# Performance work log

Hardware: AMD Instinct MI355X
Metric: run time of the kernel (lower is better)

The kernel has to match this reference:

```python
import jax, jax.numpy as jnp
import numpy as np

NUM_LOC = 20000
T = 24
IN_DIM = 18
H1 = 32
H2 = 32
GRU = 32
PW = 15
E_RAND = 640000


def setup_inputs() -> dict:
    key = jax.random.key(0)
    ks = jax.random.split(key, 32)
    # graph: random edges + self loops so every node has >=1 incoming edge
    edge_src = jnp.concatenate([
        jax.random.randint(ks[0], (E_RAND,), 0, NUM_LOC),
        jnp.arange(NUM_LOC)]).astype(jnp.int32)
    edge_dst = jnp.concatenate([
        jax.random.randint(ks[1], (E_RAND,), 0, NUM_LOC),
        jnp.arange(NUM_LOC)]).astype(jnp.int32)
    dynamic = jax.random.normal(ks[2], (NUM_LOC, T, IN_DIM), dtype=jnp.float32)
    cI = jax.random.uniform(ks[3], (T,), dtype=jnp.float32)
    cR = jax.random.uniform(ks[4], (T,), dtype=jnp.float32)
    I = jax.random.uniform(ks[5], (T,), dtype=jnp.float32)
    R = jax.random.uniform(ks[6], (T,), dtype=jnp.float32)
    N = jax.random.uniform(ks[7], (NUM_LOC, 1), dtype=jnp.float32) * 1e4 + 10.0
    h0 = jax.random.normal(ks[8], (1, GRU), dtype=jnp.float32) * 0.1
    s = 0.1
    # GAT layer 1 (torch Linear convention: weight [out, in], y = x @ W.T + b)
    W1 = jax.random.normal(ks[9], (H1, IN_DIM), dtype=jnp.float32) * s
    b1 = jnp.zeros((H1,), dtype=jnp.float32)
    aW1 = jax.random.normal(ks[10], (1, 2 * H1), dtype=jnp.float32) * s
    ab1 = jnp.zeros((1,), dtype=jnp.float32)
    # GAT layer 2
    W2 = jax.random.normal(ks[11], (H2, H1), dtype=jnp.float32) * s
    b2 = jnp.zeros((H2,), dtype=jnp.float32)
    aW2 = jax.random.normal(ks[12], (1, 2 * H2), dtype=jnp.float32) * s
    ab2 = jnp.zeros((1,), dtype=jnp.float32)
    # GRUCell
    Wih = jax.random.normal(ks[13], (3 * GRU, H2), dtype=jnp.float32) * s
    Whh = jax.random.normal(ks[14], (3 * GRU, GRU), dtype=jnp.float32) * s
    bih = jnp.zeros((3 * GRU,), dtype=jnp.float32)
    bhh = jnp.zeros((3 * GRU,), dtype=jnp.float32)
    # output heads
    WI = jax.random.normal(ks[15], (PW, GRU + 2), dtype=jnp.float32) * s
    bI = jnp.zeros((PW,), dtype=jnp.float32)
    WR = jax.random.normal(ks[16], (PW, GRU + 2), dtype=jnp.float32) * s
    bR = jnp.zeros((PW,), dtype=jnp.float32)
    Ws = jax.random.normal(ks[17], (2, GRU + 2), dtype=jnp.float32) * s
    bs = jnp.zeros((2,), dtype=jnp.float32)
    return {"dynamic": dynamic, "cI": cI, "cR": cR, "N": N, "I": I, "R": R,
            "h0": h0, "W1": W1, "b1": b1, "aW1": aW1, "ab1": ab1,
            "W2": W2, "b2": b2, "aW2": aW2, "ab2": ab2,
            "Wih": Wih, "Whh": Whh, "bih": bih, "bhh": bhh,
            "WI": WI, "bI": bI, "WR": WR, "bR": bR, "Ws": Ws, "bs": bs,
            "edge_src": edge_src, "edge_dst": edge_dst}


def _gat(x, W, b, aW, ab, src, dst):
    # z = fc(x); per-edge attention e = leaky_relu(attn_fc([z_src, z_dst]))
    z = x @ W.T + b                                        # [n, out]
    e = jax.nn.leaky_relu(
        (jnp.concatenate([z[src], z[dst]], axis=1) @ aW.T + ab)[:, 0])  # [E]
    # softmax over incoming edges per destination node
    m = jax.ops.segment_max(e, dst, num_segments=NUM_LOC)
    ex = jnp.exp(e - m[dst])
    den = jax.ops.segment_sum(ex, dst, num_segments=NUM_LOC)
    alpha = ex / den[dst]
    return jax.ops.segment_sum(alpha[:, None] * z[src], dst, num_segments=NUM_LOC)


def reference(dynamic, cI, cR, N, I, R, h0,
              W1, b1, aW1, ab1, W2, b2, aW2, ab2,
              Wih, Whh, bih, bhh, WI, bI, WR, bR, Ws, bs,
              edge_src, edge_dst):
    Nv = N[:, 0]                                          # [num_loc]

    def step(h, inp):
        x_t, cI_t, cR_t, I_t, R_t = inp
        c = jax.nn.elu(_gat(x_t, W1, b1, aW1, ab1, edge_src, edge_dst))
        c = jax.nn.elu(_gat(c, W2, b2, aW2, ab2, edge_src, edge_dst))
        pooled = jnp.max(c, axis=0)[None, :]              # [1, H2]
        # GRUCell
        gi = pooled @ Wih.T + bih
        gh = h @ Whh.T + bhh
        r = jax.nn.sigmoid(gi[:, :GRU] + gh[:, :GRU])
        zg = jax.nn.sigmoid(gi[:, GRU:2 * GRU] + gh[:, GRU:2 * GRU])
        n = jnp.tanh(gi[:, 2 * GRU:] + r * gh[:, 2 * GRU:])
        h_new = (1.0 - zg) * n + zg * h                   # [1, GRU]
        hc = jnp.concatenate([h_new, cI_t.reshape(1, 1), cR_t.reshape(1, 1)], axis=1)
        pred_I = hc @ WI.T + bI                           # [1, PW]
        pred_R = hc @ WR.T + bR
        sir = hc @ Ws.T + bs                              # [1, 2]
        alpha = jax.nn.sigmoid(sir[0, 0])
        beta = jax.nn.sigmoid(sir[0, 1])

        def sir_step(carry, _):
            lI, lR = carry
            lS = Nv - lI - lR
            dI = alpha * lI * (lS / Nv) - beta * lI
            dR = beta * lI
            return (lI + jax.lax.stop_gradient(dI),
                    lR + jax.lax.stop_gradient(dR)), (dI, dR)

        init = (jnp.broadcast_to(I_t, Nv.shape), jnp.broadcast_to(R_t, Nv.shape))
        _, (dIs, dRs) = jax.lax.scan(sir_step, init, None, length=PW)
        # [PW, num_loc] -> [num_loc, PW]
        return h_new, (pred_I, pred_R, dIs.T, dRs.T)

    xs = (jnp.swapaxes(dynamic, 0, 1), cI, cR, I, R)      # time-major
    h_fin, (nI, nR, pI, pR) = jax.lax.scan(step, h0, xs)
    new_I = jnp.transpose(nI, (1, 0, 2))                  # [1, T, PW]
    new_R = jnp.transpose(nR, (1, 0, 2))
    phy_I = jnp.transpose(pI, (1, 0, 2))                  # [num_loc, T, PW]
    phy_R = jnp.transpose(pR, (1, 0, 2))
    return new_I, new_R, phy_I, phy_R, h_fin
```

## Files before the change

kernel.cpp:

```cpp
#include <hip/hip_runtime.h>
#include <hip/hip_fp16.h>
#include <math.h>
#include <float.h>

#define NLOC 20000
#define TT   24
#define NP   12
#define INDIM 18
#define HH   32
#define PWN  15
#define PSTR 32

typedef unsigned short u16;

__device__ __forceinline__ unsigned int fkey(float f) {
    unsigned int b = __float_as_uint(f);
    return b ^ ((unsigned int)((int)b >> 31) | 0x80000000u);
}
__device__ __forceinline__ float funkey(unsigned int u) {
    return (u & 0x80000000u) ? __uint_as_float(u ^ 0x80000000u) : __uint_as_float(~u);
}

__device__ __forceinline__ bool decode_q(int nblk, int swz, int qadd,
                                         int& q, int& blk) {
    if (swz) {
        int F = blockIdx.x;
        int g = F >> 3;
        q = (F & 7) + 8 * (g / nblk);
        blk = g % nblk;
        return q < NP;
    }
    q = qadd + blockIdx.y;
    blk = blockIdx.x;
    return true;
}

__global__ void count_kernel(const int* __restrict__ dst, int* __restrict__ cnt, int E) {
    int e = blockIdx.x * blockDim.x + threadIdx.x;
    if (e < E) atomicAdd(&cnt[dst[e]], 1);
}

__global__ void scan_kernel(const int* __restrict__ cnt, int* __restrict__ row_ptr, int n) {
    __shared__ int sums[1024];
    const int CH = 20;
    int tid = threadIdx.x;
    int base = tid * CH;
    int local[CH];
    int s = 0;
    #pragma unroll
    for (int i = 0; i < CH; ++i) {
        int idx = base + i;
        int v = (idx < n) ? cnt[idx] : 0;
        local[i] = s;
        s += v;
    }
    sums[tid] = s;
    __syncthreads();
    for (int o = 1; o < 1024; o <<= 1) {
        int v = (tid >= o) ? sums[tid - o] : 0;
        __syncthreads();
        sums[tid] += v;
        __syncthreads();
    }
    int pre = (tid > 0) ? sums[tid - 1] : 0;
    #pragma unroll
    for (int i = 0; i < CH; ++i) {
        int idx = base + i;
        if (idx < n) row_ptr[idx] = pre + local[i];
    }
    if (tid == 1023) row_ptr[n] = sums[1023];
}

__global__ void scatter_kernel(const int* __restrict__ src, const int* __restrict__ dst,
                               const int* __restrict__ row_ptr, int* __restrict__ fill,
                               u16* __restrict__ csr_src, int E) {
    int e = blockIdx.x * blockDim.x + threadIdx.x;
    if (e < E) {
        int d = dst[e];
        int pos = row_ptr[d] + atomicAdd(&fill[d], 1);
        csr_src[pos] = (u16)src[e];
    }
}

__global__ void node1_kernel(const float* __restrict__ dyn,
                             const float* __restrict__ W, const float* __restrict__ b,
                             const float* __restrict__ aW, const float* __restrict__ ab,
                             __half2* __restrict__ z2, float2* __restrict__ es2,
                             float2* __restrict__ ed2, int nblk, int swz, int qadd) {
    __shared__ float sW[HH * INDIM];
    __shared__ float sb[HH];
    __shared__ float saW[2 * HH];
    __shared__ float sab;
    int q, blk;
    if (!decode_q(nblk, swz, qadd, q, blk)) return;
    int slice = swz ? q : blockIdx.y;
    int tid = threadIdx.x;
    for (int i = tid; i < HH * INDIM; i += blockDim.x) sW[i] = W[i];
    if (tid < HH) sb[tid] = b[tid];
    if (tid < 2 * HH) saW[tid] = aW[tid];
    if (tid == 0) sab = ab[0];
    __syncthreads();
    int n = blk * blockDim.x + tid;
    if (n >= NLOC) return;
    z2  += (size_t)slice * NLOC * HH;
    es2 += (size_t)slice * NLOC;
    ed2 += (size_t)slice * NLOC;
    const float* xp = dyn + (size_t)n * (TT * INDIM) + (size_t)(2 * q) * INDIM;
    float x0[INDIM], x1[INDIM];
    #pragma unroll
    for (int i = 0; i < INDIM; ++i) { x0[i] = xp[i]; x1[i] = xp[INDIM + i]; }
    float es0 = 0.f, es1 = 0.f, ed0 = sab, ed1 = sab;
    #pragma unroll
    for (int k = 0; k < HH; ++k) {
        float a0 = sb[k], a1 = sb[k];
        #pragma unroll
        for (int i = 0; i < INDIM; ++i) {
            a0 = fmaf(x0[i], sW[k * INDIM + i], a0);
            a1 = fmaf(x1[i], sW[k * INDIM + i], a1);
        }
        z2[(size_t)n * HH + k] = __floats2half2_rn(a0, a1);
        es0 = fmaf(saW[k], a0, es0);       es1 = fmaf(saW[k], a1, es1);
        ed0 = fmaf(saW[HH + k], a0, ed0);  ed1 = fmaf(saW[HH + k], a1, ed1);
    }
    es2[n] = make_float2(es0, es1);
    ed2[n] = make_float2(ed0, ed1);
}

__global__ void node2_kernel(const __half2* __restrict__ c2,
                             const float* __restrict__ W, const float* __restrict__ b,
                             const float* __restrict__ aW, const float* __restrict__ ab,
                             __half2* __restrict__ z2, float2* __restrict__ es2,
                             float2* __restrict__ ed2, int nblk, int swz, int qadd) {
    __shared__ float sW[HH * HH];
    __shared__ float sb[HH];
    __shared__ float saW[2 * HH];
    __shared__ float sab;
    int q, blk;
    if (!decode_q(nblk, swz, qadd, q, blk)) return;
    int slice = swz ? q : blockIdx.y;
    int tid = threadIdx.x;
    for (int i = tid; i < HH * HH; i += blockDim.x) sW[i] = W[i];
    if (tid < HH) sb[tid] = b[tid];
    if (tid < 2 * HH) saW[tid] = aW[tid];
    if (tid == 0) sab = ab[0];
    __syncthreads();
    int n = blk * blockDim.x + tid;
    if (n >= NLOC) return;
    c2  += (size_t)slice * NLOC * HH;
    z2  += (size_t)slice * NLOC * HH;
    es2 += (size_t)slice * NLOC;
    ed2 += (size_t)slice * NLOC;
    float x0[HH], x1[HH];
    const __half2* cp = c2 + (size_t)n * HH;
    #pragma unroll
    for (int i = 0; i < HH; ++i) {
        float2 f = __half22float2(cp[i]);
        x0[i] = f.x; x1[i] = f.y;
    }
    float es0 = 0.f, es1 = 0.f, ed0 = sab, ed1 = sab;
    #pragma unroll
    for (int k = 0; k < HH; ++k) {
        float a0 = sb[k], a1 = sb[k];
        #pragma unroll
        for (int i = 0; i < HH; ++i) {
            a0 = fmaf(x0[i], sW[k * HH + i], a0);
            a1 = fmaf(x1[i], sW[k * HH + i], a1);
        }
        z2[(size_t)n * HH + k] = __floats2half2_rn(a0, a1);
        es0 = fmaf(saW[k], a0, es0);       es1 = fmaf(saW[k], a1, es1);
        ed0 = fmaf(saW[HH + k], a0, ed0);  ed1 = fmaf(saW[HH + k], a1, ed1);
    }
    es2[n] = make_float2(es0, es1);
    ed2[n] = make_float2(ed0, ed1);
}

template<bool WRITE_C, bool POOL>
__global__ void __launch_bounds__(256, 4)
agg_kernel(const int* __restrict__ row_ptr, const u16* __restrict__ csr,
           const __half2* __restrict__ z2t, const float2* __restrict__ es2,
           const float2* __restrict__ ed2, __half2* __restrict__ c2out,
           unsigned int* __restrict__ pooled_u, int nblk, int swz, int qadd) {
    __shared__ int    soff[4][64];
    __shared__ float2 swt[4][64];
    __shared__ float  sred[4][2][HH];
    int q, dblk;
    if (!decode_q(nblk, swz, qadd, q, dblk)) return;
    int slice = swz ? q : blockIdx.y;
    int lane = threadIdx.x & 63;
    int w    = threadIdx.x >> 6;
    int r    = lane >> 3;
    int cg   = lane & 7;
    int d = dblk * 4 + w;
    const __half2* z2q  = z2t + (size_t)slice * NLOC * HH;
    const float2*  es2q = es2 + (size_t)slice * NLOC;
    const float2*  ed2q = ed2 + (size_t)slice * NLOC;

    int beg = 0, end = 0;
    float edd0 = 0.f, edd1 = 0.f;
    if (d < NLOC) {
        beg = row_ptr[d];
        end = row_ptr[d + 1];
        float2 ev = ed2q[d];
        edd0 = ev.x; edd1 = ev.y;
    }
    int deg = end - beg;
    int il = beg + lane;
    bool valid = (il < end);
    int idx_l = valid ? (int)csr[il] : 0;
    float2 esv = es2q[idx_l];
    float e0 = esv.x + edd0; e0 = fmaxf(e0, 0.01f * e0);
    float e1 = esv.y + edd1; e1 = fmaxf(e1, 0.01f * e1);
    float w0 = valid ? __expf(e0) : 0.f;
    float w1 = valid ? __expf(e1) : 0.f;
    soff[w][lane] = idx_l << 7;
    swt[w][lane]  = make_float2(w0, w1);

    const char* zb = (const char*)z2q + cg * 16;
    float2 ac0 = {0.f, 0.f}, ac1 = {0.f, 0.f}, ac2 = {0.f, 0.f}, ac3 = {0.f, 0.f};
    float den0 = 0.f, den1 = 0.f;
    #pragma unroll
    for (int pass = 0; pass < 8; ++pass) {
        int    off = soff[w][pass * 8 + r];
        float2 wv  = swt[w][pass * 8 + r];
        uint4 u = *(const uint4*)(zb + off);
        den0 += wv.x; den1 += wv.y;
        float2 f0 = __half22float2(*(const __half2*)&u.x);
        float2 f1 = __half22float2(*(const __half2*)&u.y);
        float2 f2 = __half22float2(*(const __half2*)&u.z);
        float2 f3 = __half22float2(*(const __half2*)&u.w);
        ac0.x = fmaf(wv.x, f0.x, ac0.x); ac0.y = fmaf(wv.y, f0.y, ac0.y);
        ac1.x = fmaf(wv.x, f1.x, ac1.x); ac1.y = fmaf(wv.y, f1.y, ac1.y);
        ac2.x = fmaf(wv.x, f2.x, ac2.x); ac2.y = fmaf(wv.y, f2.y, ac2.y);
        ac3.x = fmaf(wv.x, f3.x, ac3.x); ac3.y = fmaf(wv.y, f3.y, ac3.y);
    }
    for (int e = 64 + r; e < deg; e += 8) {
        int s2 = (int)csr[beg + e];
        float2 esv2 = es2q[s2];
        float t0 = esv2.x + edd0; t0 = fmaxf(t0, 0.01f * t0);
        float t1 = esv2.y + edd1; t1 = fmaxf(t1, 0.01f * t1);
        float x0 = __expf(t0), x1 = __expf(t1);
        den0 += x0; den1 += x1;
        uint4 u = *(const uint4*)(zb + ((size_t)s2 << 7));
        float2 f0 = __half22float2(*(const __half2*)&u.x);
        float2 f1 = __half22float2(*(const __half2*)&u.y);
        float2 f2 = __half22float2(*(const __half2*)&u.z);
        float2 f3 = __half22float2(*(const __half2*)&u.w);
        ac0.x = fmaf(x0, f0.x, ac0.x); ac0.y = fmaf(x1, f0.y, ac0.y);
        ac1.x = fmaf(x0, f1.x, ac1.x); ac1.y = fmaf(x1, f1.y, ac1.y);
        ac2.x = fmaf(x0, f2.x, ac2.x); ac2.y = fmaf(x1, f2.y, ac2.y);
        ac3.x = fmaf(x0, f3.x, ac3.x); ac3.y = fmaf(x1, f3.y, ac3.y);
    }
    #pragma unroll
    for (int o = 8; o <= 32; o <<= 1) {
        ac0.x += __shfl_xor(ac0.x, o, 64); ac0.y += __shfl_xor(ac0.y, o, 64);
        ac1.x += __shfl_xor(ac1.x, o, 64); ac1.y += __shfl_xor(ac1.y, o, 64);
        ac2.x += __shfl_xor(ac2.x, o, 64); ac2.y += __shfl_xor(ac2.y, o, 64);
        ac3.x += __shfl_xor(ac3.x, o, 64); ac3.y += __shfl_xor(ac3.y, o, 64);
        den0  += __shfl_xor(den0,  o, 64); den1  += __shfl_xor(den1,  o, 64);
    }

    float v00 = -FLT_MAX, v01 = -FLT_MAX, v10 = -FLT_MAX, v11 = -FLT_MAX;
    float v20 = -FLT_MAX, v21 = -FLT_MAX, v30 = -FLT_MAX, v31 = -FLT_MAX;
    if (d < NLOC) {
        float r0 = 1.f / den0, r1 = 1.f / den1;
        v00 = ac0.x * r0; v00 = fmaxf(v00, __expf(fminf(v00, 0.f)) - 1.f);
        v01 = ac0.y * r1; v01 = fmaxf(v01, __expf(fminf(v01, 0.f)) - 1.f);
        v10 = ac1.x * r0; v10 = fmaxf(v10, __expf(fminf(v10, 0.f)) - 1.f);
        v11 = ac1.y * r1; v11 = fmaxf(v11, __expf(fminf(v11, 0.f)) - 1.f);
        v20 = ac2.x * r0; v20 = fmaxf(v20, __expf(fminf(v20, 0.f)) - 1.f);
        v21 = ac2.y * r1; v21 = fmaxf(v21, __expf(fminf(v21, 0.f)) - 1.f);
        v30 = ac3.x * r0; v30 = fmaxf(v30, __expf(fminf(v30, 0.f)) - 1.f);
        v31 = ac3.y * r1; v31 = fmaxf(v31, __expf(fminf(v31, 0.f)) - 1.f);
        if (WRITE_C && r == 0) {
            uint4 pk;
            __half2 h0 = __floats2half2_rn(v00, v01);
            __half2 h1 = __floats2half2_rn(v10, v11);
            __half2 h2 = __floats2half2_rn(v20, v21);
            __half2 h3 = __floats2half2_rn(v30, v31);
            pk.x = *(unsigned int*)&h0; pk.y = *(unsigned int*)&h1;
            pk.z = *(unsigned int*)&h2; pk.w = *(unsigned int*)&h3;
            *(uint4*)((char*)(c2out + (size_t)slice * NLOC * HH + (size_t)d * HH) + cg * 16) = pk;
        }
    }
    if (POOL) {
        if (r == 0) {
            sred[w][0][cg * 4 + 0] = v00; sred[w][1][cg * 4 + 0] = v01;
            sred[w][0][cg * 4 + 1] = v10; sred[w][1][cg * 4 + 1] = v11;
            sred[w][0][cg * 4 + 2] = v20; sred[w][1][cg * 4 + 2] = v21;
            sred[w][0][cg * 4 + 3] = v30; sred[w][1][cg * 4 + 3] = v31;
        }
        __syncthreads();
        if (threadIdx.x < 64) {
            int pp = threadIdx.x >> 5;
            int dim = threadIdx.x & 31;
            float m = fmaxf(fmaxf(sred[0][pp][dim], sred[1][pp][dim]),
                            fmaxf(sred[2][pp][dim], sred[3][pp][dim]));
            atomicMax(&pooled_u[(size_t)((2 * q + pp) * HH + dim) * PSTR], fkey(m));
        }
    }
}

__global__ void gru_all_kernel(const unsigned int* __restrict__ pooled_u,
                               const float* __restrict__ Wih, const float* __restrict__ Whh,
                               const float* __restrict__ bih, const float* __restrict__ bhh,
                               const float* __restrict__ WI, const float* __restrict__ bI,
                               const float* __restrict__ WR, const float* __restrict__ bR,
                               const float* __restrict__ Ws, const float* __restrict__ bs,
                               const float* __restrict__ cIv, const float* __restrict__ cRv,
                               const float* __restrict__ h0, float* __restrict__ abArr,
                               float* __restrict__ out_newI, float* __restrict__ out_newR,
                               float* __restrict__ h_fin) {
    __shared__ float pooled[HH], hs[HH], gi[96], gh[96], hc[34];
    int tid = threadIdx.x;
    float wih_r[HH], whh_r[HH];
    if (tid < 96) {
        #pragma unroll
        for (int k = 0; k < HH; ++k) {
            wih_r[k] = Wih[tid * HH + k];
            whh_r[k] = Whh[tid * HH + k];
        }
    }
    if (tid < HH) hs[tid] = h0[tid];
    __syncthreads();
    for (int t = 0; t < TT; ++t) {
        if (tid < HH) pooled[tid] = funkey(pooled_u[(size_t)(t * HH + tid) * PSTR]);
        __syncthreads();
        if (tid < 96) {
            float a = bih[tid], g = bhh[tid];
            #pragma unroll
            for (int k = 0; k < HH; ++k) {
                a = fmaf(wih_r[k], pooled[k], a);
                g = fmaf(whh_r[k], hs[k], g);
            }
            gi[tid] = a; gh[tid] = g;
        }
        __syncthreads();
        if (tid < HH) {
            float r  = 1.f / (1.f + expf(-(gi[tid] + gh[tid])));
            float zg = 1.f / (1.f + expf(-(gi[HH + tid] + gh[HH + tid])));
            float nn = tanhf(gi[2 * HH + tid] + r * gh[2 * HH + tid]);
            float hn = (1.f - zg) * nn + zg * hs[tid];
            hs[tid] = hn;
            hc[tid] = hn;
        }
        if (tid == 32) hc[32] = cIv[t];
        if (tid == 33) hc[33] = cRv[t];
        __syncthreads();
        if (tid < PWN) {
            float a = bI[tid];
            #pragma unroll
            for (int k = 0; k < 34; ++k) a = fmaf(WI[tid * 34 + k], hc[k], a);
            out_newI[t * PWN + tid] = a;
        } else if (tid >= 32 && tid < 32 + PWN) {
            int p = tid - 32;
            float a = bR[p];
            #pragma unroll
            for (int k = 0; k < 34; ++k) a = fmaf(WR[p * 34 + k], hc[k], a);
            out_newR[t * PWN + p] = a;
        } else if (tid == 64 || tid == 65) {
            int p = tid - 64;
            float a = bs[p];
            #pragma unroll
            for (int k = 0; k < 34; ++k) a = fmaf(Ws[p * 34 + k], hc[k], a);
            abArr[2 * t + p] = 1.f / (1.f + expf(-a));
        }
        __syncthreads();
    }
    if (tid < HH) h_fin[tid] = hs[tid];
}

__global__ void sir_kernel(const float* __restrict__ Nin, const float* __restrict__ Iv,
                           const float* __restrict__ Rv, const float* __restrict__ abArr,
                           float* __restrict__ phyI, float* __restrict__ phyR) {
    int idx = blockIdx.x * blockDim.x + threadIdx.x;
    if (idx >= NLOC * TT) return;
    int n = idx / TT, t = idx - n * TT;
    float Nv = Nin[n];
    float alpha = abArr[2 * t], beta = abArr[2 * t + 1];
    float lI = Iv[t], lR = Rv[t];
    float* oI = phyI + (size_t)idx * PWN;
    float* oR = phyR + (size_t)idx * PWN;
    #pragma unroll
    for (int p = 0; p < PWN; ++p) {
        float lS = Nv - lI - lR;
        float dI = alpha * lI * (lS / Nv) - beta * lI;
        float dR = beta * lI;
        oI[p] = dI;
        oR[p] = dR;
        lI += dI;
        lR += dR;
    }
}

extern "C" void kernel_launch(void* const* d_in, const int* in_sizes, int n_in,
                              void* d_out, int out_size, void* d_ws, size_t ws_size,
                              hipStream_t stream) {
    const float* dynamic = (const float*)d_in[0];
    const float* cIv = (const float*)d_in[1];
    const float* cRv = (const float*)d_in[2];
    const float* Nin = (const float*)d_in[3];
    const float* Iv  = (const float*)d_in[4];
    const float* Rv  = (const float*)d_in[5];
    const float* h0  = (const float*)d_in[6];
    const float* W1  = (const float*)d_in[7];
    const float* b1  = (const float*)d_in[8];
    const float* aW1 = (const float*)d_in[9];
    const float* ab1 = (const float*)d_in[10];
    const float* W2  = (const float*)d_in[11];
    const float* b2  = (const float*)d_in[12];
    const float* aW2 = (const float*)d_in[13];
    const float* ab2 = (const float*)d_in[14];
    const float* Wih = (const float*)d_in[15];
    const float* Whh = (const float*)d_in[16];
    const float* bih = (const float*)d_in[17];
    const float* bhh = (const float*)d_in[18];
    const float* WI  = (const float*)d_in[19];
    const float* bI  = (const float*)d_in[20];
    const float* WR  = (const float*)d_in[21];
    const float* bR  = (const float*)d_in[22];
    const float* Ws  = (const float*)d_in[23];
    const float* bs  = (const float*)d_in[24];
    const int* esrc  = (const int*)d_in[25];
    const int* edst  = (const int*)d_in[26];
    const int E = in_sizes[25];

    float* out = (float*)d_out;
    float* out_newI = out;
    float* out_newR = out + TT * PWN;
    float* phyI = out + 2 * TT * PWN;
    float* phyR = phyI + (size_t)NLOC * TT * PWN;
    float* h_fin = phyR + (size_t)NLOC * TT * PWN;

    char* p = (char*)d_ws;
    int* cnt = (int*)p;                 p += (size_t)NLOC * 4;
    int* fill = (int*)p;                p += (size_t)NLOC * 4;
    int* row_ptr = (int*)p;             p += (size_t)(NLOC + 2) * 4;
    u16* csr = (u16*)p;                 p += ((size_t)E * 2 + 15) & ~(size_t)15;
    unsigned int* pooled_u = (unsigned int*)p; p += (size_t)TT * HH * PSTR * 4;
    float* abArr = (float*)p;           p += (size_t)2 * TT * 4;
    p = (char*)(((size_t)p + 127) & ~(size_t)127);
    size_t fixed_bytes = (size_t)(p - (char*)d_ws);
    size_t per_q_bytes = (size_t)NLOC * HH * 4 * 2 + (size_t)NLOC * 8 * 2;
    int B = 1;
    if (ws_size > fixed_bytes + per_q_bytes)
        B = (int)((ws_size - fixed_bytes) / per_q_bytes);
    if (B > NP) B = NP;
    if (B < 1) B = 1;
    __half2* zb  = (__half2*)p;
    __half2* cb  = zb + (size_t)B * NLOC * HH;
    float2* es2  = (float2*)(cb + (size_t)B * NLOC * HH);
    float2* ed2  = es2 + (size_t)B * NLOC;

    hipMemsetAsync(cnt, 0, (size_t)2 * NLOC * 4, stream);
    hipMemsetAsync(pooled_u, 0, (size_t)TT * HH * PSTR * 4, stream);

    int egrid = (E + 255) / 256;
    count_kernel<<<egrid, 256, 0, stream>>>(edst, cnt, E);
    scan_kernel<<<1, 1024, 0, stream>>>(cnt, row_ptr, NLOC);
    scatter_kernel<<<egrid, 256, 0, stream>>>(esrc, edst, row_ptr, fill, csr, E);

    const int NBLK_N = (NLOC + 255) / 256;
    const int NBLK_A = (NLOC + 3) / 4;

    if (B >= NP) {
        dim3 ng(NBLK_N * 16), ag(NBLK_A * 16);
        node1_kernel<<<ng, 256, 0, stream>>>(dynamic, W1, b1, aW1, ab1,
                                             zb, es2, ed2, NBLK_N, 1, 0);
        agg_kernel<true, false><<<ag, 256, 0, stream>>>(
            row_ptr, csr, zb, es2, ed2, cb, pooled_u, NBLK_A, 1, 0);
        node2_kernel<<<ng, 256, 0, stream>>>(cb, W2, b2, aW2, ab2,
                                             zb, es2, ed2, NBLK_N, 1, 0);
        agg_kernel<false, true><<<ag, 256, 0, stream>>>(
            row_ptr, csr, zb, es2, ed2, nullptr, pooled_u, NBLK_A, 1, 0);
    } else {
        for (int qbase = 0; qbase < NP; qbase += B) {
            int Bc = NP - qbase; if (Bc > B) Bc = B;
            dim3 ng(NBLK_N, Bc), ag(NBLK_A, Bc);
            node1_kernel<<<ng, 256, 0, stream>>>(dynamic, W1, b1, aW1, ab1,
                                                 zb, es2, ed2, NBLK_N, 0, qbase);
            agg_kernel<true, false><<<ag, 256, 0, stream>>>(
                row_ptr, csr, zb, es2, ed2, cb, pooled_u, NBLK_A, 0, qbase);
            node2_kernel<<<ng, 256, 0, stream>>>(cb, W2, b2, aW2, ab2,
                                                 zb, es2, ed2, NBLK_N, 0, qbase);
            agg_kernel<false, true><<<ag, 256, 0, stream>>>(
                row_ptr, csr, zb, es2, ed2, nullptr, pooled_u, NBLK_A, 0, qbase);
        }
    }

    gru_all_kernel<<<1, 128, 0, stream>>>(pooled_u, Wih, Whh, bih, bhh,
                                          WI, bI, WR, bR, Ws, bs, cIv, cRv,
                                          h0, abArr, out_newI, out_newR, h_fin);
    sir_kernel<<<(NLOC * TT + 255) / 256, 256, 0, stream>>>(Nin, Iv, Rv, abArr, phyI, phyR);
}
```

Baseline: 637.8 us.

## Rebalance swizzled grid to drop idle blocks and batch gather loads in aggregation

The swizzled block mapping no longer pads twelve time-pairs up to sixteen. Eight pairs get one full block row and the last four share half-rows, so the grid holds fewer dead blocks. In agg_kernel the per-edge offset and weights are packed into one int4 shared stage, and all eight neighbor z loads are issued before the FMAs to raise memory-level parallelism. The launch bounds drop from 4 to 2 blocks per CU to make room for the extra registers, which risks lower occupancy. Dead blocks now stay alive through the barriers and skip their work with a flag.

```diff
diff --git a/kernel.cpp b/kernel.cpp
--- a/kernel.cpp
+++ b/kernel.cpp
@@ -21,14 +21,17 @@
     return (u & 0x80000000u) ? __uint_as_float(u ^ 0x80000000u) : __uint_as_float(~u);
 }
 
-__device__ __forceinline__ bool decode_q(int nblk, int swz, int qadd,
-                                         int& q, int& blk) {
+__device__ __forceinline__ bool decode_bal(int nblk, int half, int swz, int qadd,
+                                           int& q, int& blk) {
     if (swz) {
         int F = blockIdx.x;
+        int x = F & 7;
         int g = F >> 3;
-        q = (F & 7) + 8 * (g / nblk);
-        blk = g % nblk;
-        return q < NP;
+        if (g < nblk) { q = x; blk = g; return true; }
+        int h = g - nblk;
+        q = 8 + (x >> 1);
+        blk = (x & 1) * half + h;
+        return blk < nblk;
     }
     q = qadd + blockIdx.y;
     blk = blockIdx.x;
@@ -86,13 +89,13 @@
                              const float* __restrict__ W, const float* __restrict__ b,
                              const float* __restrict__ aW, const float* __restrict__ ab,
                              __half2* __restrict__ z2, float2* __restrict__ es2,
-                             float2* __restrict__ ed2, int nblk, int swz, int qadd) {
+                             float2* __restrict__ ed2, int nblk, int half, int swz, int qadd) {
     __shared__ float sW[HH * INDIM];
     __shared__ float sb[HH];
     __shared__ float saW[2 * HH];
     __shared__ float sab;
     int q, blk;
-    if (!decode_q(nblk, swz, qadd, q, blk)) return;
+    bool alive = decode_bal(nblk, half, swz, qadd, q, blk);
     int slice = swz ? q : blockIdx.y;
     int tid = threadIdx.x;
     for (int i = tid; i < HH * INDIM; i += blockDim.x) sW[i] = W[i];
@@ -100,6 +103,7 @@
     if (tid < 2 * HH) saW[tid] = aW[tid];
     if (tid == 0) sab = ab[0];
     __syncthreads();
+    if (!alive) return;
     int n = blk * blockDim.x + tid;
     if (n >= NLOC) return;
     z2  += (size_t)slice * NLOC * HH;
@@ -130,13 +134,13 @@
                              const float* __restrict__ W, const float* __restrict__ b,
                              const float* __restrict__ aW, const float* __restrict__ ab,
                              __half2* __restrict__ z2, float2* __restrict__ es2,
-                             float2* __restrict__ ed2, int nblk, int swz, int qadd) {
+                             float2* __restrict__ ed2, int nblk, int half, int swz, int qadd) {
     __shared__ float sW[HH * HH];
     __shared__ float sb[HH];
     __shared__ float saW[2 * HH];
     __shared__ float sab;
     int q, blk;
-    if (!decode_q(nblk, swz, qadd, q, blk)) return;
+    bool alive = decode_bal(nblk, half, swz, qadd, q, blk);
     int slice = swz ? q : blockIdx.y;
     int tid = threadIdx.x;
     for (int i = tid; i < HH * HH; i += blockDim.x) sW[i] = W[i];
@@ -144,6 +148,7 @@
     if (tid < 2 * HH) saW[tid] = aW[tid];
     if (tid == 0) sab = ab[0];
     __syncthreads();
+    if (!alive) return;
     int n = blk * blockDim.x + tid;
     if (n >= NLOC) return;
     c2  += (size_t)slice * NLOC * HH;
@@ -175,16 +180,15 @@
 }
 
 template<bool WRITE_C, bool POOL>
-__global__ void __launch_bounds__(256, 4)
+__global__ void __launch_bounds__(256, 2)
 agg_kernel(const int* __restrict__ row_ptr, const u16* __restrict__ csr,
            const __half2* __restrict__ z2t, const float2* __restrict__ es2,
            const float2* __restrict__ ed2, __half2* __restrict__ c2out,
-           unsigned int* __restrict__ pooled_u, int nblk, int swz, int qadd) {
-    __shared__ int    soff[4][64];
-    __shared__ float2 swt[4][64];
-    __shared__ float  sred[4][2][HH];
+           unsigned int* __restrict__ pooled_u, int nblk, int half, int swz, int qadd) {
+    __shared__ int4  sstage[4][64];
+    __shared__ float sred[4][2][HH];
     int q, dblk;
-    if (!decode_q(nblk, swz, qadd, q, dblk)) return;
+    bool alive = decode_bal(nblk, half, swz, qadd, q, dblk);
     int slice = swz ? q : blockIdx.y;
     int lane = threadIdx.x & 63;
     int w    = threadIdx.x >> 6;
@@ -195,102 +199,108 @@
     const float2*  es2q = es2 + (size_t)slice * NLOC;
     const float2*  ed2q = ed2 + (size_t)slice * NLOC;
 
-    int beg = 0, end = 0;
-    float edd0 = 0.f, edd1 = 0.f;
-    if (d < NLOC) {
-        beg = row_ptr[d];
-        end = row_ptr[d + 1];
-        float2 ev = ed2q[d];
-        edd0 = ev.x; edd1 = ev.y;
-    }
-    int deg = end - beg;
-    int il = beg + lane;
-    bool valid = (il < end);
-    int idx_l = valid ? (int)csr[il] : 0;
-    float2 esv = es2q[idx_l];
-    float e0 = esv.x + edd0; e0 = fmaxf(e0, 0.01f * e0);
-    float e1 = esv.y + edd1; e1 = fmaxf(e1, 0.01f * e1);
-    float w0 = valid ? __expf(e0) : 0.f;
-    float w1 = valid ? __expf(e1) : 0.f;
-    soff[w][lane] = idx_l << 7;
-    swt[w][lane]  = make_float2(w0, w1);
-
-    const char* zb = (const char*)z2q + cg * 16;
-    float2 ac0 = {0.f, 0.f}, ac1 = {0.f, 0.f}, ac2 = {0.f, 0.f}, ac3 = {0.f, 0.f};
-    float den0 = 0.f, den1 = 0.f;
-    #pragma unroll
-    for (int pass = 0; pass < 8; ++pass) {
-        int    off = soff[w][pass * 8 + r];
-        float2 wv  = swt[w][pass * 8 + r];
-        uint4 u = *(const uint4*)(zb + off);
-        den0 += wv.x; den1 += wv.y;
-        float2 f0 = __half22float2(*(const __half2*)&u.x);
-        float2 f1 = __half22float2(*(const __half2*)&u.y);
-        float2 f2 = __half22float2(*(const __half2*)&u.z);
-        float2 f3 = __half22float2(*(const __half2*)&u.w);
-        ac0.x = fmaf(wv.x, f0.x, ac0.x); ac0.y = fmaf(wv.y, f0.y, ac0.y);
-        ac1.x = fmaf(wv.x, f1.x, ac1.x); ac1.y = fmaf(wv.y, f1.y, ac1.y);
-        ac2.x = fmaf(wv.x, f2.x, ac2.x); ac2.y = fmaf(wv.y, f2.y, ac2.y);
-        ac3.x = fmaf(wv.x, f3.x, ac3.x); ac3.y = fmaf(wv.y, f3.y, ac3.y);
-    }
-    for (int e = 64 + r; e < deg; e += 8) {
-        int s2 = (int)csr[beg + e];
-        float2 esv2 = es2q[s2];
-        float t0 = esv2.x + edd0; t0 = fmaxf(t0, 0.01f * t0);
-        float t1 = esv2.y + edd1; t1 = fmaxf(t1, 0.01f * t1);
-        float x0 = __expf(t0), x1 = __expf(t1);
-        den0 += x0; den1 += x1;
-        uint4 u = *(const uint4*)(zb + ((size_t)s2 << 7));
-        float2 f0 = __half22float2(*(const __half2*)&u.x);
-        float2 f1 = __half22float2(*(const __half2*)&u.y);
-        float2 f2 = __half22float2(*(const __half2*)&u.z);
-        float2 f3 = __half22float2(*(const __half2*)&u.w);
-        ac0.x = fmaf(x0, f0.x, ac0.x); ac0.y = fmaf(x1, f0.y, ac0.y);
-        ac1.x = fmaf(x0, f1.x, ac1.x); ac1.y = fmaf(x1, f1.y, ac1.y);
-        ac2.x = fmaf(x0, f2.x, ac2.x); ac2.y = fmaf(x1, f2.y, ac2.y);
-        ac3.x = fmaf(x0, f3.x, ac3.x); ac3.y = fmaf(x1, f3.y, ac3.y);
-    }
-    #pragma unroll
-    for (int o = 8; o <= 32; o <<= 1) {
-        ac0.x += __shfl_xor(ac0.x, o, 64); ac0.y += __shfl_xor(ac0.y, o, 64);
-        ac1.x += __shfl_xor(ac1.x, o, 64); ac1.y += __shfl_xor(ac1.y, o, 64);
-        ac2.x += __shfl_xor(ac2.x, o, 64); ac2.y += __shfl_xor(ac2.y, o, 64);
-        ac3.x += __shfl_xor(ac3.x, o, 64); ac3.y += __shfl_xor(ac3.y, o, 64);
-        den0  += __shfl_xor(den0,  o, 64); den1  += __shfl_xor(den1,  o, 64);
-    }
-
     float v00 = -FLT_MAX, v01 = -FLT_MAX, v10 = -FLT_MAX, v11 = -FLT_MAX;
     float v20 = -FLT_MAX, v21 = -FLT_MAX, v30 = -FLT_MAX, v31 = -FLT_MAX;
-    if (d < NLOC) {
-        float r0 = 1.f / den0, r1 = 1.f / den1;
-        v00 = ac0.x * r0; v00 = fmaxf(v00, __expf(fminf(v00, 0.f)) - 1.f);
-        v01 = ac0.y * r1; v01 = fmaxf(v01, __expf(fminf(v01, 0.f)) - 1.f);
-        v10 = ac1.x * r0; v10 = fmaxf(v10, __expf(fminf(v10, 0.f)) - 1.f);
-        v11 = ac1.y * r1; v11 = fmaxf(v11, __expf(fminf(v11, 0.f)) - 1.f);
-        v20 = ac2.x * r0; v20 = fmaxf(v20, __expf(fminf(v20, 0.f)) - 1.f);
-        v21 = ac2.y * r1; v21 = fmaxf(v21, __expf(fminf(v21, 0.f)) - 1.f);
-        v30 = ac3.x * r0; v30 = fmaxf(v30, __expf(fminf(v30, 0.f)) - 1.f);
-        v31 = ac3.y * r1; v31 = fmaxf(v31, __expf(fminf(v31, 0.f)) - 1.f);
-        if (WRITE_C && r == 0) {
-            uint4 pk;
-            __half2 h0 = __floats2half2_rn(v00, v01);
-            __half2 h1 = __floats2half2_rn(v10, v11);
-            __half2 h2 = __floats2half2_rn(v20, v21);
-            __half2 h3 = __floats2half2_rn(v30, v31);
-            pk.x = *(unsigned int*)&h0; pk.y = *(unsigned int*)&h1;
-            pk.z = *(unsigned int*)&h2; pk.w = *(unsigned int*)&h3;
-            *(uint4*)((char*)(c2out + (size_t)slice * NLOC * HH + (size_t)d * HH) + cg * 16) = pk;
+
+    if (alive) {
+        int beg = 0, end = 0;
+        float edd0 = 0.f, edd1 = 0.f;
+        if (d < NLOC) {
+            beg = row_ptr[d];
+            end = row_ptr[d + 1];
+            float2 ev = ed2q[d];
+            edd0 = ev.x; edd1 = ev.y;
+        }
+        int deg = end - beg;
+        int il = beg + lane;
+        bool valid = (il < end);
+        int idx_l = valid ? (int)csr[il] : 0;
+        float2 esv = es2q[idx_l];
+        float e0 = esv.x + edd0; e0 = fmaxf(e0, 0.01f * e0);
+        float e1 = esv.y + edd1; e1 = fmaxf(e1, 0.01f * e1);
+        float w0 = valid ? __expf(e0) : 0.f;
+        float w1 = valid ? __expf(e1) : 0.f;
+        sstage[w][lane] = make_int4(idx_l << 7, __float_as_int(w0), __float_as_int(w1), 0);
+
+        const char* zb = (const char*)z2q + cg * 16;
+        int4 st[8];
+        #pragma unroll
+        for (int i = 0; i < 8; ++i) st[i] = sstage[w][i * 8 + r];
+        uint4 zl[8];
+        #pragma unroll
+        for (int i = 0; i < 8; ++i) zl[i] = *(const uint4*)(zb + st[i].x);
+        float2 ac0 = {0.f, 0.f}, ac1 = {0.f, 0.f}, ac2 = {0.f, 0.f}, ac3 = {0.f, 0.f};
+        float den0 = 0.f, den1 = 0.f;
+        #pragma unroll
+        for (int i = 0; i < 8; ++i) {
+            float wx = __int_as_float(st[i].y), wy = __int_as_float(st[i].z);
+            den0 += wx; den1 += wy;
+            float2 f0 = __half22float2(*(const __half2*)&zl[i].x);
+            float2 f1 = __half22float2(*(const __half2*)&zl[i].y);
+            float2 f2 = __half22float2(*(const __half2*)&zl[i].z);
+            float2 f3 = __half22float2(*(const __half2*)&zl[i].w);
+            ac0.x = fmaf(wx, f0.x, ac0.x); ac0.y = fmaf(wy, f0.y, ac0.y);
+            ac1.x = fmaf(wx, f1.x, ac1.x); ac1.y = fmaf(wy, f1.y, ac1.y);
+            ac2.x = fmaf(wx, f2.x, ac2.x); ac2.y = fmaf(wy, f2.y, ac2.y);
+            ac3.x = fmaf(wx, f3.x, ac3.x); ac3.y = fmaf(wy, f3.y, ac3.y);
+        }
+        for (int e = 64 + r; e < deg; e += 8) {
+            int s2 = (int)csr[beg + e];
+            float2 esv2 = es2q[s2];
+            float t0 = esv2.x + edd0; t0 = fmaxf(t0, 0.01f * t0);
+            float t1 = esv2.y + edd1; t1 = fmaxf(t1, 0.01f * t1);
+            float x0 = __expf(t0), x1 = __expf(t1);
+            den0 += x0; den1 += x1;
+            uint4 u = *(const uint4*)(zb + ((size_t)s2 << 7));
+            float2 f0 = __half22float2(*(const __half2*)&u.x);
+            float2 f1 = __half22float2(*(const __half2*)&u.y);
+            float2 f2 = __half22float2(*(const __half2*)&u.z);
+            float2 f3 = __half22float2(*(const __half2*)&u.w);
+            ac0.x = fmaf(x0, f0.x, ac0.x); ac0.y = fmaf(x1, f0.y, ac0.y);
+            ac1.x = fmaf(x0, f1.x, ac1.x); ac1.y = fmaf(x1, f1.y, ac1.y);
+            ac2.x = fmaf(x0, f2.x, ac2.x); ac2.y = fmaf(x1, f2.y, ac2.y);
+            ac3.x = fmaf(x0, f3.x, ac3.x); ac3.y = fmaf(x1, f3.y, ac3.y);
+        }
+        #pragma unroll
+        for (int o = 8; o <= 32; o <<= 1) {
+            ac0.x += __shfl_xor(ac0.x, o, 64); ac0.y += __shfl_xor(ac0.y, o, 64);
+            ac1.x += __shfl_xor(ac1.x, o, 64); ac1.y += __shfl_xor(ac1.y, o, 64);
+            ac2.x += __shfl_xor(ac2.x, o, 64); ac2.y += __shfl_xor(ac2.y, o, 64);
+            ac3.x += __shfl_xor(ac3.x, o, 64); ac3.y += __shfl_xor(ac3.y, o, 64);
+            den0  += __shfl_xor(den0,  o, 64); den1  += __shfl_xor(den1,  o, 64);
+        }
+
+        if (d < NLOC) {
+            float r0 = 1.f / den0, r1 = 1.f / den1;
+            v00 = ac0.x * r0; v00 = fmaxf(v00, __expf(fminf(v00, 0.f)) - 1.f);
+            v01 = ac0.y * r1; v01 = fmaxf(v01, __expf(fminf(v01, 0.f)) - 1.f);
+            v10 = ac1.x * r0; v10 = fmaxf(v10, __expf(fminf(v10, 0.f)) - 1.f);
+            v11 = ac1.y * r1; v11 = fmaxf(v11, __expf(fminf(v11, 0.f)) - 1.f);
+            v20 = ac2.x * r0; v20 = fmaxf(v20, __expf(fminf(v20, 0.f)) - 1.f);
+            v21 = ac2.y * r1; v21 = fmaxf(v21, __expf(fminf(v21, 0.f)) - 1.f);
+            v30 = ac3.x * r0; v30 = fmaxf(v30, __expf(fminf(v30, 0.f)) - 1.f);
+            v31 = ac3.y * r1; v31 = fmaxf(v31, __expf(fminf(v31, 0.f)) - 1.f);
+            if (WRITE_C && r == 0) {
+                uint4 pk;
+                __half2 h0 = __floats2half2_rn(v00, v01);
+                __half2 h1 = __floats2half2_rn(v10, v11);
+                __half2 h2 = __floats2half2_rn(v20, v21);
+                __half2 h3 = __floats2half2_rn(v30, v31);
+                pk.x = *(unsigned int*)&h0; pk.y = *(unsigned int*)&h1;
+                pk.z = *(unsigned int*)&h2; pk.w = *(unsigned int*)&h3;
+                *(uint4*)((char*)(c2out + (size_t)slice * NLOC * HH + (size_t)d * HH) + cg * 16) = pk;
+            }
         }
     }
     if (POOL) {
-        if (r == 0) {
+        if (alive && r == 0) {
             sred[w][0][cg * 4 + 0] = v00; sred[w][1][cg * 4 + 0] = v01;
             sred[w][0][cg * 4 + 1] = v10; sred[w][1][cg * 4 + 1] = v11;
             sred[w][0][cg * 4 + 2] = v20; sred[w][1][cg * 4 + 2] = v21;
             sred[w][0][cg * 4 + 3] = v30; sred[w][1][cg * 4 + 3] = v31;
         }
         __syncthreads();
-        if (threadIdx.x < 64) {
+        if (alive && threadIdx.x < 64) {
             int pp = threadIdx.x >> 5;
             int dim = threadIdx.x & 31;
             float m = fmaxf(fmaxf(sred[0][pp][dim], sred[1][pp][dim]),
@@ -461,29 +471,31 @@
 
     const int NBLK_N = (NLOC + 255) / 256;
     const int NBLK_A = (NLOC + 3) / 4;
+    const int HALF_N = (NBLK_N + 1) / 2;
+    const int HALF_A = (NBLK_A + 1) / 2;
 
     if (B >= NP) {
-        dim3 ng(NBLK_N * 16), ag(NBLK_A * 16);
+        dim3 ng(8 * (NBLK_N + HALF_N)), ag(8 * (NBLK_A + HALF_A));
         node1_kernel<<<ng, 256, 0, stream>>>(dynamic, W1, b1, aW1, ab1,
-                                             zb, es2, ed2, NBLK_N, 1, 0);
+                                             zb, es2, ed2, NBLK_N, HALF_N, 1, 0);
         agg_kernel<true, false><<<ag, 256, 0, stream>>>(
-            row_ptr, csr, zb, es2, ed2, cb, pooled_u, NBLK_A, 1, 0);
+            row_ptr, csr, zb, es2, ed2, cb, pooled_u, NBLK_A, HALF_A, 1, 0);
         node2_kernel<<<ng, 256, 0, stream>>>(cb, W2, b2, aW2, ab2,
-                                             zb, es2, ed2, NBLK_N, 1, 0);
+                                             zb, es2, ed2, NBLK_N, HALF_N, 1, 0);
         agg_kernel<false, true><<<ag, 256, 0, stream>>>(
-            row_ptr, csr, zb, es2, ed2, nullptr, pooled_u, NBLK_A, 1, 0);
+            row_ptr, csr, zb, es2, ed2, nullptr, pooled_u, NBLK_A, HALF_A, 1, 0);
     } else {
         for (int qbase = 0; qbase < NP; qbase += B) {
             int Bc = NP - qbase; if (Bc > B) Bc = B;
             dim3 ng(NBLK_N, Bc), ag(NBLK_A, Bc);
             node1_kernel<<<ng, 256, 0, stream>>>(dynamic, W1, b1, aW1, ab1,
-                                                 zb, es2, ed2, NBLK_N, 0, qbase);
+                                                 zb, es2, ed2, NBLK_N, HALF_N, 0, qbase);
             agg_kernel<true, false><<<ag, 256, 0, stream>>>(
-                row_ptr, csr, zb, es2, ed2, cb, pooled_u, NBLK_A, 0, qbase);
+                row_ptr, csr, zb, es2, ed2, cb, pooled_u, NBLK_A, HALF_A, 0, qbase);
             node2_kernel<<<ng, 256, 0, stream>>>(cb, W2, b2, aW2, ab2,
-                                                 zb, es2, ed2, NBLK_N, 0, qbase);
+                                                 zb, es2, ed2, NBLK_N, HALF_N, 0, qbase);
             agg_kernel<false, true><<<ag, 256, 0, stream>>>(
-                row_ptr, csr, zb, es2, ed2, nullptr, pooled_u, NBLK_A, 0, qbase);
+                row_ptr, csr, zb, es2, ed2, nullptr, pooled_u, NBLK_A, HALF_A, 0, qbase);
         }
     }
 
```

Result: slower. 667.1 us (+4.6%).
